# Optimization experiments

Measured on AMD Instinct MI355X. Metric: run time of the kernel, lower is better.

The kernel has to match this reference:

```python
import jax, jax.numpy as jnp
import numpy as np

B, N_ENT, E, T, DEPTH, N_TREES = 512, 2000, 512, 512, 6, 2
N_LEAVES = 2 ** DEPTH  # 64


def setup_inputs() -> dict:
    key = jax.random.key(0)
    ks = jax.random.split(key, 20)
    s = lambda fan_in: 1.0 / np.sqrt(fan_in)
    inp = {
        "leaf_idx": jax.random.randint(ks[0], (B, N_TREES, N_LEAVES), 0, N_ENT),
        "ent_emb": jax.random.normal(ks[1], (N_ENT, E), jnp.float32),
        "th_emb": jax.random.normal(ks[2], (T,), jnp.float32),
        # two2one: Linear(2E,4E) ReLU Linear(4E,E) ReLU
        "w1": jax.random.normal(ks[3], (2 * E, 4 * E), jnp.float32) * s(2 * E),
        "b1": jnp.zeros((4 * E,), jnp.float32),
        "w2": jax.random.normal(ks[4], (4 * E, E), jnp.float32) * s(4 * E),
        "b2": jnp.zeros((E,), jnp.float32),
        # one2one: Linear(E,4E) ReLU Linear(4E,E) Tanh
        "o1": jax.random.normal(ks[5], (E, 4 * E), jnp.float32) * s(E),
        "ob1": jnp.zeros((4 * E,), jnp.float32),
        "o2": jax.random.normal(ks[6], (4 * E, E), jnp.float32) * s(4 * E),
        "ob2": jnp.zeros((E,), jnp.float32),
        # theorem head: (T + 2E) -> E -> E/2 -> E/4 -> 1
        "h1": jax.random.normal(ks[7], (T + N_TREES * E, E), jnp.float32) * s(T + N_TREES * E),
        "hb1": jnp.zeros((E,), jnp.float32),
        "h2": jax.random.normal(ks[8], (E, E // 2), jnp.float32) * s(E),
        "hb2": jnp.zeros((E // 2,), jnp.float32),
        "h3": jax.random.normal(ks[9], (E // 2, E // 4), jnp.float32) * s(E // 2),
        "hb3": jnp.zeros((E // 4,), jnp.float32),
        "h4": jax.random.normal(ks[10], (E // 4, 1), jnp.float32) * s(E // 4),
        "hb4": jnp.zeros((1,), jnp.float32),
    }
    return inp


def _two2one(x, w1, b1, w2, b2):
    # x: [..., n_pairs, 2E] -> [..., n_pairs, E]  (ReLU, ReLU)
    h = jax.nn.relu(x @ w1 + b1)
    return jax.nn.relu(h @ w2 + b2)


def _one2one(x, o1, ob1, o2, ob2):
    # ReLU then Tanh, as in one2one_layers
    h = jax.nn.relu(x @ o1 + ob1)
    return jnp.tanh(h @ o2 + ob2)


def reference(leaf_idx, ent_emb, th_emb, w1, b1, w2, b2, o1, ob1, o2, ob2,
              h1, hb1, h2, hb2, h3, hb3, h4, hb4):
    # Leaf embedding lookups: [B, N_TREES, N_LEAVES, E]
    x = ent_emb[leaf_idx]
    # Level-by-level binary tree reduction with the two2one MLP
    n = N_LEAVES
    while n > 1:
        x = x.reshape(B, N_TREES, n // 2, 2 * E)
        x = _two2one(x, w1, b1, w2, b2)
        n //= 2
    root = x.reshape(B, N_TREES, E)
    # Unary numerical function applied at each entity root (Tanh output)
    root = _one2one(root, o1, ob1, o2, ob2)
    # Theorem head: concat theorem embedding with the entity encodings
    feat = jnp.concatenate(
        [jnp.broadcast_to(th_emb, (B, T)), root.reshape(B, N_TREES * E)], axis=-1)
    z = jax.nn.relu(feat @ h1 + hb1)
    z = jax.nn.relu(z @ h2 + hb2)
    z = jax.nn.relu(z @ h3 + hb3)
    return jax.nn.sigmoid(z @ h4 + hb4)  # [B, 1]
```

## Files before the change

kernel.cpp:

```cpp
#include <hip/hip_runtime.h>
#include <cstddef>
#include <cstdint>


typedef _Float16 f16;
typedef _Float16 f16x8 __attribute__((ext_vector_type(8)));
typedef float f32x4 __attribute__((ext_vector_type(4)));

__device__ __forceinline__ void gll16(const void* g, void* l) {
  __builtin_amdgcn_global_load_lds(
      (const __attribute__((address_space(1))) void*)g,
      (__attribute__((address_space(3))) void*)l, 16, 0, 0);
}

template <int ACT, int OUTF32, int GATHER>
__global__ __launch_bounds__(256) void gemm_f16(
    const f16* __restrict__ A, const f16* __restrict__ Bt,
    const float* __restrict__ bias, void* __restrict__ Cout, int N, int K,
    const int* __restrict__ lidx, const f16* __restrict__ entf) {
  __shared__ __align__(16) f16 As[128 * 64];
  __shared__ __align__(16) f16 Bs[128 * 64];
  const int tid = threadIdx.x;
  const int m0 = blockIdx.y * 128;
  const int n0 = blockIdx.x * 128;

  const int srow = tid >> 3;
  const int sk = ((tid & 7) ^ ((tid >> 3) & 7)) << 3;
  const f16* Ag = A + (size_t)(m0 + srow) * K + sk;
  const f16* Bg = Bt + (size_t)(n0 + srow) * K + sk;
  char* Al = (char*)As + (tid >> 6) * 1024;
  char* Bl = (char*)Bs + (tid >> 6) * 1024;

  int ent0[4], ent1[4];
  if (GATHER) {
#pragma unroll
    for (int r = 0; r < 4; ++r) {
      const int row2 = (m0 + srow + 32 * r) << 1;
      ent0[r] = lidx[row2];
      ent1[r] = lidx[row2 + 1];
    }
  }

  const int l = tid & 63;
  const int wm = tid >> 7;
  const int wn = (tid >> 6) & 1;
  const int q = l & 15;
  const int kg = l >> 4;
  const char* Ar = (const char*)As + (wm * 64 + q) * 128;
  const char* Br = (const char*)Bs + (wn * 64 + q) * 128;
  const int c0 = ((kg << 4) ^ ((q & 7) << 4));

  f32x4 acc[4][4] = {};

  for (int k0 = 0; k0 < K; k0 += 64) {
    if (GATHER) {
      const int h = k0 >> 9;
      const int kk = (k0 & 511) + sk;
#pragma unroll
      for (int r = 0; r < 4; ++r) {
        const int e = h ? ent1[r] : ent0[r];
        gll16(entf + ((size_t)e << 9) + kk, Al + r * 4096);
        gll16(Bg + (size_t)(r * 32) * K + k0, Bl + r * 4096);
      }
    } else {
#pragma unroll
      for (int r = 0; r < 4; ++r) {
        gll16(Ag + (size_t)(r * 32) * K + k0, Al + r * 4096);
        gll16(Bg + (size_t)(r * 32) * K + k0, Bl + r * 4096);
      }
    }
    __syncthreads();
#pragma unroll
    for (int ks = 0; ks < 2; ++ks) {
      const int cb = c0 ^ (ks << 6);
      f16x8 a[4], b[4];
#pragma unroll
      for (int i = 0; i < 4; ++i) a[i] = *(const f16x8*)(Ar + i * 2048 + cb);
#pragma unroll
      for (int j = 0; j < 4; ++j) b[j] = *(const f16x8*)(Br + j * 2048 + cb);
#pragma unroll
      for (int i = 0; i < 4; ++i)
#pragma unroll
        for (int j = 0; j < 4; ++j)
          acc[i][j] = __builtin_amdgcn_mfma_f32_16x16x32_f16(a[i], b[j],
                                                             acc[i][j], 0, 0, 0);
    }
    __syncthreads();
  }

#pragma unroll
  for (int j = 0; j < 4; ++j) {
    const int col = n0 + wn * 64 + j * 16 + q;
    const float bsv = bias[col];
#pragma unroll
    for (int i = 0; i < 4; ++i) {
      f32x4 v = acc[i][j];
#pragma unroll
      for (int vi = 0; vi < 4; ++vi) {
        const int row = m0 + wm * 64 + i * 16 + kg * 4 + vi;
        float c = v[vi] + bsv;
        if (ACT == 1) c = fmaxf(c, 0.0f);
        if (ACT == 2) c = tanhf(c);
        if (OUTF32)
          ((float*)Cout)[(size_t)row * N + col] = c;
        else
          ((f16*)Cout)[(size_t)row * N + col] = (f16)c;
      }
    }
  }
}

__global__ void transpose_cvt(const float* __restrict__ src,
                              f16* __restrict__ dst, int K, int N) {
  __shared__ f16 tile[32][33];
  const int k0 = blockIdx.x * 32, n0 = blockIdx.y * 32;
  const int tx = threadIdx.x & 31, ty = threadIdx.x >> 5;
  for (int r = ty; r < 32; r += 8)
    tile[r][tx] = (f16)src[(size_t)(k0 + r) * N + n0 + tx];
  __syncthreads();
  for (int r = ty; r < 32; r += 8)
    dst[(size_t)(n0 + r) * K + k0 + tx] = tile[tx][r];
}

__global__ void cvt_f16(const float* __restrict__ src, f16* __restrict__ dst) {
  const int g = blockIdx.x * 256 + threadIdx.x;
  const float4* s = (const float4*)(src + (size_t)g * 8);
  float4 v0 = s[0], v1 = s[1];
  f16x8 o;
  o[0] = (f16)v0.x; o[1] = (f16)v0.y; o[2] = (f16)v0.z; o[3] = (f16)v0.w;
  o[4] = (f16)v1.x; o[5] = (f16)v1.y; o[6] = (f16)v1.z; o[7] = (f16)v1.w;
  *(f16x8*)(dst + (size_t)g * 8) = o;
}

__global__ void build_feat_h(const float* __restrict__ th,
                             const f16* __restrict__ root,
                             f16* __restrict__ feat) {
  int idx = blockIdx.x * 256 + threadIdx.x;
  int b = idx / 1536;
  int c = idx - b * 1536;
  feat[idx] = (c < 512) ? (f16)th[c] : root[(size_t)b * 1024 + (c - 512)];
}

__global__ void head_final(const float* __restrict__ z3,
                           const float* __restrict__ h4,
                           const float* __restrict__ hb4,
                           float* __restrict__ out) {
  int row = blockIdx.x;
  int t = threadIdx.x;
  float v = z3[(size_t)row * 128 + t] * h4[t] +
            z3[(size_t)row * 128 + 64 + t] * h4[64 + t];
#pragma unroll
  for (int off = 32; off; off >>= 1) v += __shfl_down(v, off);
  if (t == 0) out[row] = 1.0f / (1.0f + expf(-(v + hb4[0])));
}

extern "C" void kernel_launch(void* const* d_in, const int* in_sizes, int n_in,
                              void* d_out, int out_size, void* d_ws,
                              size_t ws_size, hipStream_t stream) {
  const int* leaf_idx = (const int*)d_in[0];
  const float* ent_emb = (const float*)d_in[1];
  const float* th_emb = (const float*)d_in[2];
  const float* w1 = (const float*)d_in[3];
  const float* b1 = (const float*)d_in[4];
  const float* w2 = (const float*)d_in[5];
  const float* b2 = (const float*)d_in[6];
  const float* o1 = (const float*)d_in[7];
  const float* ob1 = (const float*)d_in[8];
  const float* o2 = (const float*)d_in[9];
  const float* ob2 = (const float*)d_in[10];
  const float* h1 = (const float*)d_in[11];
  const float* hb1 = (const float*)d_in[12];
  const float* h2 = (const float*)d_in[13];
  const float* hb2 = (const float*)d_in[14];
  const float* h3 = (const float*)d_in[15];
  const float* hb3 = (const float*)d_in[16];
  const float* h4 = (const float*)d_in[17];
  const float* hb4 = (const float*)d_in[18];
  float* out = (float*)d_out;

  char* p = (char*)d_ws;
  f16* w1t = (f16*)p;  p += (size_t)2048 * 1024 * 2;
  f16* w2t = (f16*)p;  p += (size_t)512 * 2048 * 2;
  f16* o1t = (f16*)p;  p += (size_t)2048 * 512 * 2;
  f16* o2t = (f16*)p;  p += (size_t)512 * 2048 * 2;
  f16* h1t = (f16*)p;  p += (size_t)512 * 1536 * 2;
  f16* h2t = (f16*)p;  p += (size_t)256 * 512 * 2;
  f16* h3t = (f16*)p;  p += (size_t)128 * 256 * 2;
  f16* entf = (f16*)p; p += (size_t)2000 * 512 * 2;
  f16* bufA = (f16*)p; p += (size_t)32768 * 512 * 2;
  f16* bufB = (f16*)p; p += (size_t)16384 * 512 * 2;
  f16* Hf   = (f16*)p; p += (size_t)16384 * 2048 * 2;
  f16* featf = (f16*)p; p += (size_t)512 * 1536 * 2;
  f16* z1h  = (f16*)p; p += (size_t)512 * 512 * 2;
  f16* z2h  = (f16*)p; p += (size_t)512 * 256 * 2;
  float* z3 = (float*)p; p += (size_t)512 * 128 * 4;

  transpose_cvt<<<dim3(1024 / 32, 2048 / 32), 256, 0, stream>>>(w1, w1t, 1024, 2048);
  transpose_cvt<<<dim3(2048 / 32, 512 / 32), 256, 0, stream>>>(w2, w2t, 2048, 512);
  transpose_cvt<<<dim3(512 / 32, 2048 / 32), 256, 0, stream>>>(o1, o1t, 512, 2048);
  transpose_cvt<<<dim3(2048 / 32, 512 / 32), 256, 0, stream>>>(o2, o2t, 2048, 512);
  transpose_cvt<<<dim3(1536 / 32, 512 / 32), 256, 0, stream>>>(h1, h1t, 1536, 512);
  transpose_cvt<<<dim3(512 / 32, 256 / 32), 256, 0, stream>>>(h2, h2t, 512, 256);
  transpose_cvt<<<dim3(256 / 32, 128 / 32), 256, 0, stream>>>(h3, h3t, 256, 128);
  cvt_f16<<<(2000 * 512) / 2048, 256, 0, stream>>>(ent_emb, entf);

  const f16* inb = nullptr;
  int pairs = 32;
  const int CHUNK = 16384;
  for (int level = 0; level < 6; ++level) {
    int M = 1024 * pairs;
    f16* outb = (level & 1) ? bufB : bufA;
    for (int r0 = 0; r0 < M; r0 += CHUNK) {
      int rows = (M - r0) < CHUNK ? (M - r0) : CHUNK;
      if (level == 0) {
        gemm_f16<1, 0, 1><<<dim3(2048 / 128, rows / 128), 256, 0, stream>>>(
            nullptr, w1t, b1, Hf, 2048, 1024, leaf_idx + (size_t)2 * r0, entf);
      } else {
        gemm_f16<1, 0, 0><<<dim3(2048 / 128, rows / 128), 256, 0, stream>>>(
            inb + (size_t)r0 * 1024, w1t, b1, Hf, 2048, 1024, nullptr, nullptr);
      }
      gemm_f16<1, 0, 0><<<dim3(512 / 128, rows / 128), 256, 0, stream>>>(
          Hf, w2t, b2, outb + (size_t)r0 * 512, 512, 2048, nullptr, nullptr);
    }
    inb = outb;
    pairs >>= 1;
  }

  gemm_f16<1, 0, 0><<<dim3(2048 / 128, 1024 / 128), 256, 0, stream>>>(
      inb, o1t, ob1, Hf, 2048, 512, nullptr, nullptr);
  f16* rootf = bufA;
  gemm_f16<2, 0, 0><<<dim3(512 / 128, 1024 / 128), 256, 0, stream>>>(
      Hf, o2t, ob2, rootf, 512, 2048, nullptr, nullptr);

  build_feat_h<<<(512 * 1536) / 256, 256, 0, stream>>>(th_emb, rootf, featf);
  gemm_f16<1, 0, 0><<<dim3(512 / 128, 512 / 128), 256, 0, stream>>>(
      featf, h1t, hb1, z1h, 512, 1536, nullptr, nullptr);
  gemm_f16<1, 0, 0><<<dim3(256 / 128, 512 / 128), 256, 0, stream>>>(
      z1h, h2t, hb2, z2h, 256, 512, nullptr, nullptr);
  gemm_f16<1, 1, 0><<<dim3(128 / 128, 512 / 128), 256, 0, stream>>>(
      z2h, h3t, hb3, z3, 128, 256, nullptr, nullptr);
  head_final<<<512, 64, 0, stream>>>(z3, h4, hb4, out);
}
```

Before: 888.7 us.

## Add 256x256 double-buffered 8-wave GEMM for large tree levels, drop chunking

Adds a 512-thread GEMM kernel with 256x256 tiles, double-buffered LDS staging interleaved with MFMA phases, partial vmcnt waits and wave priority hints. It is used for the large first-level GEMMs, including the gathered leaf level. The row chunking is removed by enlarging the hidden buffer so each level runs as a single launch. The aim is higher arithmetic intensity and overlap of loads with compute on the dominant GEMMs, at the cost of more workspace memory and heavier register and LDS use per block.

```diff
diff --git a/kernel.cpp b/kernel.cpp
--- a/kernel.cpp
+++ b/kernel.cpp
@@ -13,34 +13,162 @@
       (__attribute__((address_space(3))) void*)l, 16, 0, 0);
 }
 
-template <int ACT, int OUTF32, int GATHER>
-__global__ __launch_bounds__(256) void gemm_f16(
+#define BAR __builtin_amdgcn_s_barrier()
+#define VM6 asm volatile("s_waitcnt vmcnt(6)" ::: "memory")
+#define VM0 asm volatile("s_waitcnt vmcnt(0)" ::: "memory")
+
+template <int GATHER>
+__global__ __launch_bounds__(512) void gemm8(
     const f16* __restrict__ A, const f16* __restrict__ Bt,
-    const float* __restrict__ bias, void* __restrict__ Cout, int N, int K,
+    const float* __restrict__ bias, f16* __restrict__ C, int N, int K,
     const int* __restrict__ lidx, const f16* __restrict__ entf) {
+  __shared__ __align__(16) f16 As[2][2][128][64];
+  __shared__ __align__(16) f16 Bs[2][2][128][64];
+  const int tid = threadIdx.x;
+  const int m0 = blockIdx.y * 256;
+  const int n0 = blockIdx.x * 256;
+
+  const int srow = tid >> 3;
+  const int sk = ((tid & 7) ^ (srow & 7)) << 3;
+  const int wvb = (tid >> 6) * 1024;
+  const f16* Asrc = GATHER ? (const f16*)nullptr
+                           : (A + (size_t)(m0 + srow) * K + sk);
+  const f16* Bsrc = Bt + (size_t)(n0 + srow) * K + sk;
+
+  int eA0[2][2], eA1[2][2];
+  if (GATHER) {
+#pragma unroll
+    for (int hh = 0; hh < 2; ++hh)
+#pragma unroll
+      for (int oo = 0; oo < 2; ++oo) {
+        const int grow = m0 + hh * 128 + oo * 64 + srow;
+        eA0[hh][oo] = lidx[2 * grow];
+        eA1[hh][oo] = lidx[2 * grow + 1];
+      }
+  }
+
+#define STAGE_A(BUF, HALF, KB)                                          \
+  {                                                                     \
+    char* d_ = (char*)&As[BUF][HALF][0][0] + wvb;                       \
+    if (!GATHER) {                                                      \
+      const f16* s_ = Asrc + (size_t)((HALF)*128) * K + (KB);           \
+      gll16(s_, d_);                                                    \
+      gll16(s_ + (size_t)64 * K, d_ + 8192);                            \
+    } else {                                                            \
+      const int hs_ = (KB) >> 9;                                        \
+      const int kk_ = ((KB)&511) + sk;                                  \
+      const int e0_ = hs_ ? eA1[HALF][0] : eA0[HALF][0];                \
+      const int e1_ = hs_ ? eA1[HALF][1] : eA0[HALF][1];                \
+      gll16(entf + ((size_t)e0_ << 9) + kk_, d_);                       \
+      gll16(entf + ((size_t)e1_ << 9) + kk_, d_ + 8192);                \
+    }                                                                   \
+  }
+#define STAGE_B(BUF, HALF, KB)                                          \
+  {                                                                     \
+    char* d_ = (char*)&Bs[BUF][HALF][0][0] + wvb;                       \
+    const f16* s_ = Bsrc + (size_t)((HALF)*128) * K + (KB);             \
+    gll16(s_, d_);                                                      \
+    gll16(s_ + (size_t)64 * K, d_ + 8192);                              \
+  }
+
+  const int l = tid & 63, wid = tid >> 6;
+  const int wm = wid >> 2, wn = wid & 3;
+  const int q = l & 15, kg = l >> 4;
+  const char* Ard = (const char*)&As[0][wm][0][0] + q * 128;
+  const char* Brd = (const char*)&Bs[0][wn >> 1][0][0] + ((wn & 1) * 64 + q) * 128;
+  const int csw = (kg << 4) ^ ((q & 7) << 4);
+
+  f16x8 a[8][2], b[4][2];
+  f32x4 acc[8][4] = {};
+
+#define RD_AB(BUF)                                                          \
+  {                                                                         \
+    _Pragma("unroll") for (int i_ = 0; i_ < 8; ++i_) {                      \
+      a[i_][0] = *(const f16x8*)(Ard + (BUF)*32768 + i_ * 2048 + csw);      \
+      a[i_][1] = *(const f16x8*)(Ard + (BUF)*32768 + i_ * 2048 + (csw ^ 64)); \
+    }                                                                       \
+    _Pragma("unroll") for (int j_ = 0; j_ < 4; ++j_) {                      \
+      b[j_][0] = *(const f16x8*)(Brd + (BUF)*32768 + j_ * 2048 + csw);      \
+      b[j_][1] = *(const f16x8*)(Brd + (BUF)*32768 + j_ * 2048 + (csw ^ 64)); \
+    }                                                                       \
+  }
+#define MM(MLO, KS)                                                         \
+  __builtin_amdgcn_s_setprio(1);                                            \
+  {                                                                         \
+    _Pragma("unroll") for (int i_ = 0; i_ < 4; ++i_) {                      \
+      _Pragma("unroll") for (int j_ = 0; j_ < 4; ++j_) {                    \
+        acc[(MLO)*4 + i_][j_] = __builtin_amdgcn_mfma_f32_16x16x32_f16(     \
+            a[(MLO)*4 + i_][KS], b[j_][KS], acc[(MLO)*4 + i_][j_], 0, 0, 0); \
+      }                                                                     \
+    }                                                                       \
+  }                                                                         \
+  __builtin_amdgcn_s_setprio(0);
+
+  STAGE_A(0, 0, 0); STAGE_A(0, 1, 0); STAGE_B(0, 0, 0); STAGE_B(0, 1, 0);
+  STAGE_A(1, 0, 64); STAGE_A(1, 1, 64); STAGE_B(1, 0, 64);
+  VM6; BAR;
+
+  const int niter = K >> 7;
+  int kb = 0;
+  for (int it = 0; it < niter - 1; ++it, kb += 128) {
+    const int t1 = kb + 64, t2 = kb + 128, t3 = kb + 192;
+    RD_AB(0); STAGE_B(1, 1, t1);      BAR; MM(0, 0); BAR;
+    STAGE_A(0, 0, t2);                BAR; MM(1, 0); BAR;
+    STAGE_A(0, 1, t2);                BAR; MM(0, 1); BAR;
+    STAGE_B(0, 0, t2);           VM6; BAR; MM(1, 1); BAR;
+    RD_AB(1); STAGE_B(0, 1, t2);      BAR; MM(0, 0); BAR;
+    STAGE_A(1, 0, t3);                BAR; MM(1, 0); BAR;
+    STAGE_A(1, 1, t3);                BAR; MM(0, 1); BAR;
+    STAGE_B(1, 0, t3);           VM6; BAR; MM(1, 1); BAR;
+  }
+  {
+    const int t1 = kb + 64;
+    RD_AB(0); STAGE_B(1, 1, t1);      BAR; MM(0, 0); BAR;
+                                      BAR; MM(1, 0); BAR;
+                                      BAR; MM(0, 1); BAR;
+                                 VM0; BAR; MM(1, 1); BAR;
+    RD_AB(1);                         BAR; MM(0, 0); BAR;
+                                      BAR; MM(1, 0); BAR;
+                                      BAR; MM(0, 1); BAR;
+                                      BAR; MM(1, 1); BAR;
+  }
+#undef STAGE_A
+#undef STAGE_B
+#undef RD_AB
+#undef MM
+
+#pragma unroll
+  for (int j = 0; j < 4; ++j) {
+    const int col = n0 + wn * 64 + j * 16 + q;
+    const float bsv = bias[col];
+#pragma unroll
+    for (int i = 0; i < 8; ++i) {
+      f32x4 v = acc[i][j];
+#pragma unroll
+      for (int vi = 0; vi < 4; ++vi) {
+        const int row = m0 + wm * 128 + i * 16 + kg * 4 + vi;
+        float c = fmaxf(v[vi] + bsv, 0.0f);
+        C[(size_t)row * N + col] = (f16)c;
+      }
+    }
+  }
+}
+
+template <int ACT, int OUTF32>
+__global__ __launch_bounds__(256) void gemm128(
+    const f16* __restrict__ A, const f16* __restrict__ Bt,
+    const float* __restrict__ bias, void* __restrict__ Cout, int N, int K) {
   __shared__ __align__(16) f16 As[128 * 64];
   __shared__ __align__(16) f16 Bs[128 * 64];
   const int tid = threadIdx.x;
   const int m0 = blockIdx.y * 128;
   const int n0 = blockIdx.x * 128;
-
   const int srow = tid >> 3;
   const int sk = ((tid & 7) ^ ((tid >> 3) & 7)) << 3;
   const f16* Ag = A + (size_t)(m0 + srow) * K + sk;
   const f16* Bg = Bt + (size_t)(n0 + srow) * K + sk;
   char* Al = (char*)As + (tid >> 6) * 1024;
   char* Bl = (char*)Bs + (tid >> 6) * 1024;
-
-  int ent0[4], ent1[4];
-  if (GATHER) {
-#pragma unroll
-    for (int r = 0; r < 4; ++r) {
-      const int row2 = (m0 + srow + 32 * r) << 1;
-      ent0[r] = lidx[row2];
-      ent1[r] = lidx[row2 + 1];
-    }
-  }
-
   const int l = tid & 63;
   const int wm = tid >> 7;
   const int wn = (tid >> 6) & 1;
@@ -49,25 +177,12 @@
   const char* Ar = (const char*)As + (wm * 64 + q) * 128;
   const char* Br = (const char*)Bs + (wn * 64 + q) * 128;
   const int c0 = ((kg << 4) ^ ((q & 7) << 4));
-
   f32x4 acc[4][4] = {};
-
   for (int k0 = 0; k0 < K; k0 += 64) {
-    if (GATHER) {
-      const int h = k0 >> 9;
-      const int kk = (k0 & 511) + sk;
-#pragma unroll
-      for (int r = 0; r < 4; ++r) {
-        const int e = h ? ent1[r] : ent0[r];
-        gll16(entf + ((size_t)e << 9) + kk, Al + r * 4096);
-        gll16(Bg + (size_t)(r * 32) * K + k0, Bl + r * 4096);
-      }
-    } else {
-#pragma unroll
-      for (int r = 0; r < 4; ++r) {
-        gll16(Ag + (size_t)(r * 32) * K + k0, Al + r * 4096);
-        gll16(Bg + (size_t)(r * 32) * K + k0, Bl + r * 4096);
-      }
+#pragma unroll
+    for (int r = 0; r < 4; ++r) {
+      gll16(Ag + (size_t)(r * 32) * K + k0, Al + r * 4096);
+      gll16(Bg + (size_t)(r * 32) * K + k0, Bl + r * 4096);
     }
     __syncthreads();
 #pragma unroll
@@ -87,7 +202,6 @@
     }
     __syncthreads();
   }
-
 #pragma unroll
   for (int j = 0; j < 4; ++j) {
     const int col = n0 + wn * 64 + j * 16 + q;
@@ -187,13 +301,13 @@
   f16* h2t = (f16*)p;  p += (size_t)256 * 512 * 2;
   f16* h3t = (f16*)p;  p += (size_t)128 * 256 * 2;
   f16* entf = (f16*)p; p += (size_t)2000 * 512 * 2;
+  f16* Hf   = (f16*)p; p += (size_t)32768 * 2048 * 2;
   f16* bufA = (f16*)p; p += (size_t)32768 * 512 * 2;
-  f16* bufB = (f16*)p; p += (size_t)16384 * 512 * 2;
-  f16* Hf   = (f16*)p; p += (size_t)16384 * 2048 * 2;
   f16* featf = (f16*)p; p += (size_t)512 * 1536 * 2;
   f16* z1h  = (f16*)p; p += (size_t)512 * 512 * 2;
   f16* z2h  = (f16*)p; p += (size_t)512 * 256 * 2;
   float* z3 = (float*)p; p += (size_t)512 * 128 * 4;
+  f16* bufB = Hf + (size_t)32 * 1024 * 1024;
 
   transpose_cvt<<<dim3(1024 / 32, 2048 / 32), 256, 0, stream>>>(w1, w1t, 1024, 2048);
   transpose_cvt<<<dim3(2048 / 32, 512 / 32), 256, 0, stream>>>(w2, w2t, 2048, 512);
@@ -204,40 +318,29 @@
   transpose_cvt<<<dim3(256 / 32, 128 / 32), 256, 0, stream>>>(h3, h3t, 256, 128);
   cvt_f16<<<(2000 * 512) / 2048, 256, 0, stream>>>(ent_emb, entf);
 
-  const f16* inb = nullptr;
-  int pairs = 32;
-  const int CHUNK = 16384;
-  for (int level = 0; level < 6; ++level) {
-    int M = 1024 * pairs;
-    f16* outb = (level & 1) ? bufB : bufA;
-    for (int r0 = 0; r0 < M; r0 += CHUNK) {
-      int rows = (M - r0) < CHUNK ? (M - r0) : CHUNK;
-      if (level == 0) {
-        gemm_f16<1, 0, 1><<<dim3(2048 / 128, rows / 128), 256, 0, stream>>>(
-            nullptr, w1t, b1, Hf, 2048, 1024, leaf_idx + (size_t)2 * r0, entf);
-      } else {
-        gemm_f16<1, 0, 0><<<dim3(2048 / 128, rows / 128), 256, 0, stream>>>(
-            inb + (size_t)r0 * 1024, w1t, b1, Hf, 2048, 1024, nullptr, nullptr);
-      }
-      gemm_f16<1, 0, 0><<<dim3(512 / 128, rows / 128), 256, 0, stream>>>(
-          Hf, w2t, b2, outb + (size_t)r0 * 512, 512, 2048, nullptr, nullptr);
-    }
-    inb = outb;
-    pairs >>= 1;
-  }
-
-  gemm_f16<1, 0, 0><<<dim3(2048 / 128, 1024 / 128), 256, 0, stream>>>(
-      inb, o1t, ob1, Hf, 2048, 512, nullptr, nullptr);
-  f16* rootf = bufA;
-  gemm_f16<2, 0, 0><<<dim3(512 / 128, 1024 / 128), 256, 0, stream>>>(
-      Hf, o2t, ob2, rootf, 512, 2048, nullptr, nullptr);
-
-  build_feat_h<<<(512 * 1536) / 256, 256, 0, stream>>>(th_emb, rootf, featf);
-  gemm_f16<1, 0, 0><<<dim3(512 / 128, 512 / 128), 256, 0, stream>>>(
-      featf, h1t, hb1, z1h, 512, 1536, nullptr, nullptr);
-  gemm_f16<1, 0, 0><<<dim3(256 / 128, 512 / 128), 256, 0, stream>>>(
-      z1h, h2t, hb2, z2h, 256, 512, nullptr, nullptr);
-  gemm_f16<1, 1, 0><<<dim3(128 / 128, 512 / 128), 256, 0, stream>>>(
-      z2h, h3t, hb3, z3, 128, 256, nullptr, nullptr);
+  gemm8<1><<<dim3(8, 128), 512, 0, stream>>>(nullptr, w1t, b1, Hf, 2048, 1024,
+                                             leaf_idx, entf);
+  gemm8<0><<<dim3(2, 128), 512, 0, stream>>>(Hf, w2t, b2, bufA, 512, 2048,
+                                             nullptr, nullptr);
+  gemm8<0><<<dim3(8, 64), 512, 0, stream>>>(bufA, w1t, b1, Hf, 2048, 1024,
+                                            nullptr, nullptr);
+  gemm128<1, 0><<<dim3(4, 128), 256, 0, stream>>>(Hf, w2t, b2, bufB, 512, 2048);
+  gemm8<0><<<dim3(8, 32), 512, 0, stream>>>(bufB, w1t, b1, Hf, 2048, 1024,
+                                            nullptr, nullptr);
+  gemm128<1, 0><<<dim3(4, 64), 256, 0, stream>>>(Hf, w2t, b2, bufA, 512, 2048);
+  gemm128<1, 0><<<dim3(16, 32), 256, 0, stream>>>(bufA, w1t, b1, Hf, 2048, 1024);
+  gemm128<1, 0><<<dim3(4, 32), 256, 0, stream>>>(Hf, w2t, b2, bufB, 512, 2048);
+  gemm128<1, 0><<<dim3(16, 16), 256, 0, stream>>>(bufB, w1t, b1, Hf, 2048, 1024);
+  gemm128<1, 0><<<dim3(4, 16), 256, 0, stream>>>(Hf, w2t, b2, bufA, 512, 2048);
+  gemm128<1, 0><<<dim3(16, 8), 256, 0, stream>>>(bufA, w1t, b1, Hf, 2048, 1024);
+  gemm128<1, 0><<<dim3(4, 8), 256, 0, stream>>>(Hf, w2t, b2, bufB, 512, 2048);
+
+  gemm128<1, 0><<<dim3(16, 8), 256, 0, stream>>>(bufB, o1t, ob1, Hf, 2048, 512);
+  gemm128<2, 0><<<dim3(4, 8), 256, 0, stream>>>(Hf, o2t, ob2, bufA, 512, 2048);
+
+  build_feat_h<<<(512 * 1536) / 256, 256, 0, stream>>>(th_emb, bufA, featf);
+  gemm128<1, 0><<<dim3(4, 4), 256, 0, stream>>>(featf, h1t, hb1, z1h, 512, 1536);
+  gemm128<1, 0><<<dim3(2, 4), 256, 0, stream>>>(z1h, h2t, hb2, z2h, 256, 512);
+  gemm128<1, 1><<<dim3(1, 4), 256, 0, stream>>>(z2h, h3t, hb3, z3, 128, 256);
   head_final<<<512, 64, 0, stream>>>(z3, h4, hb4, out);
 }
```

Result: slower. 989.9 us (+11.4%).
